# Kernel optimization log

Measured on AMD Instinct MI355X. Metric: run time of the kernel, lower is better.

## Reference

```python
import jax, jax.numpy as jnp
import numpy as np

B, F0, F1, E, C = 256, 39, 39, 16, 1  # batch, feature_nums[0], feature_nums[1], emb_size, w_channels
_ROWS, _COLS = np.tril_indices(F1, k=-1)  # strict lower triangle of (F1, F0); row-major order matches masked_select
I = _ROWS.shape[0]  # interaction_num = 741
BN_EPS = 1e-5


def setup_inputs() -> dict:
    key = jax.random.key(0)
    k1, k2, k3 = jax.random.split(key, 3)
    xi = jax.random.normal(k1, (B, F0, E), dtype=jnp.float32)
    xj = jax.random.normal(k2, (B, F1, E), dtype=jnp.float32)
    # W param is (1,1,C,E,E) in torch; keep the broadcastable core (C,E,E). Xavier-uniform bound.
    bound = float(np.sqrt(6.0 / (E + E)))
    W = jax.random.uniform(k3, (C, E, E), dtype=jnp.float32, minval=-bound, maxval=bound)
    gamma = jnp.ones((I,), dtype=jnp.float32)   # BatchNorm2d weight
    beta = jnp.zeros((I,), dtype=jnp.float32)   # BatchNorm2d bias
    return {"xi": xi, "xj": xj, "W": W, "gamma": gamma, "beta": beta}


def reference(xi, xj, W, gamma, beta):
    rows = jnp.asarray(_ROWS)
    cols = jnp.asarray(_COLS)
    # raw_cross[b,f1,f0,e1,e2] = xj[b,f1,e1] * xi[b,f0,e2]; only keep strict-lower-tri (f1,f0) pairs.
    # Compute triangular pairs directly instead of materializing the full (B,F1,F0,E,E) tensor.
    cross = xj[:, rows, :, None] * xi[:, cols, None, :]  # (B, I, E, E)
    # BatchNorm2d (training-mode batch stats, biased variance) over channels I
    mean = jnp.mean(cross, axis=(0, 2, 3), keepdims=True)            # (1, I, 1, 1)
    var = jnp.mean(jnp.square(cross - mean), axis=(0, 2, 3), keepdims=True)
    normed = (cross - mean) * jax.lax.rsqrt(var + BN_EPS)
    normed = normed * gamma[None, :, None, None] + beta[None, :, None, None]
    # broadcast multiply with W over w_channels, then transpose(1,2)
    out = normed[:, :, None, :, :] * W[None, None, :, :, :]          # (B, I, C, E, E)
    return jnp.transpose(out, (0, 2, 1, 3, 4))                        # (B, C, I, E, E)
```

## Files before the change

kernel.cpp:

```cpp
#include <hip/hip_runtime.h>
#include <math.h>

#define BB 256
#define FF 39
#define EE 16
#define II 741
#define BN_EPS 1e-5f
#define CPW 8
#define NB 4

typedef float vfloat4 __attribute__((ext_vector_type(4)));
typedef float vfloat2 __attribute__((ext_vector_type(2)));

struct OffTab { unsigned int v[II]; };
static constexpr OffTab make_off() {
    OffTab t{};
    int i = 0;
    for (int r = 1; r < FF; ++r)
        for (int c = 0; c < r; ++c) {
            t.v[i] = ((unsigned)(r * EE) << 16) | (unsigned)(c * EE);
            ++i;
        }
    return t;
}
__constant__ OffTab g_off = make_off();


__global__ __launch_bounds__(256) void
stats_kernel(const float* __restrict__ xi,
             const float* __restrict__ xj,
             const float* __restrict__ gamma,
             const float* __restrict__ beta,
             float* __restrict__ ws) {
    int wid = (blockIdx.x * blockDim.x + threadIdx.x) >> 6;
    int lane = threadIdx.x & 63;
    if (wid >= II) return;
    int i = wid;
    unsigned o = g_off.v[i];
    int joff = (int)(o >> 16);
    int coff = (int)(o & 0xffffu);

    float sumS = 0.f, sumQ = 0.f;
#pragma unroll
    for (int b = lane; b < BB; b += 64) {
        const vfloat4* xjr = reinterpret_cast<const vfloat4*>(xj + b * FF * EE + joff);
        const vfloat4* xic = reinterpret_cast<const vfloat4*>(xi + b * FF * EE + coff);
        float sj = 0.f, qj = 0.f, si = 0.f, qi = 0.f;
#pragma unroll
        for (int k = 0; k < 4; ++k) {
            vfloat4 vj = xjr[k];
            vfloat4 vi = xic[k];
            sj += vj.x + vj.y + vj.z + vj.w;
            qj += vj.x * vj.x + vj.y * vj.y + vj.z * vj.z + vj.w * vj.w;
            si += vi.x + vi.y + vi.z + vi.w;
            qi += vi.x * vi.x + vi.y * vi.y + vi.z * vi.z + vi.w * vi.w;
        }
        sumS += sj * si;
        sumQ += qj * qi;
    }
#pragma unroll
    for (int off = 32; off > 0; off >>= 1) {
        sumS += __shfl_xor(sumS, off);
        sumQ += __shfl_xor(sumQ, off);
    }
    if (lane == 0) {
        const float invN = 1.0f / (float)(BB * EE * EE);
        float mean = sumS * invN;
        float ex2 = sumQ * invN;
        float var = ex2 - mean * mean;
        float inv_std = 1.0f / sqrtf(var + BN_EPS);
        float a = gamma[i] * inv_std;
        float d = beta[i] - mean * a;
        vfloat2 e;
        e.x = a; e.y = d;
        reinterpret_cast<vfloat2*>(ws)[i] = e;
    }
}

__global__ __launch_bounds__(256) void
cross_bn_kernel(const float* __restrict__ xi,
                const float* __restrict__ xj,
                const float* __restrict__ W,
                const float* __restrict__ ws,
                float* __restrict__ out) {
    const vfloat2* T2 = reinterpret_cast<const vfloat2*>(ws);

    int t = threadIdx.x;
    int l = t & 63;
    int e1 = l >> 2;
    int e2q = l & 3;
    int wv = t >> 6;

    vfloat4 w4 = reinterpret_cast<const vfloat4*>(W)[e1 * 4 + e2q];

    int ibase = __builtin_amdgcn_readfirstlane(blockIdx.x * (4 * CPW) + wv * CPW);
    int b0 = blockIdx.y * NB;

    if (ibase + CPW <= II) {
        int joff[CPW], coff[CPW];
        float a[CPW], d[CPW];
#pragma unroll
        for (int k = 0; k < CPW; ++k) {
            unsigned o = g_off.v[ibase + k];
            joff[k] = (int)(o >> 16);
            coff[k] = (int)(o & 0xffffu);
            vfloat2 ad = T2[ibase + k];
            a[k] = ad.x; d[k] = ad.y;
        }
#pragma unroll
        for (int bb = 0; bb < NB; ++bb) {
            int b = b0 + bb;
            const float* xib = xi + b * FF * EE;
            const float* xjb = xj + b * FF * EE;
            float* outb = out + (size_t)b * (II * EE * EE) + (size_t)ibase * (EE * EE);
            float xjs[CPW];
            vfloat4 xi4[CPW];
#pragma unroll
            for (int k = 0; k < CPW; ++k) {
                xjs[k] = xjb[joff[k] + e1];
                xi4[k] = reinterpret_cast<const vfloat4*>(xib + coff[k])[e2q];
            }
#pragma unroll
            for (int k = 0; k < CPW; ++k) {
                vfloat4 o4;
                o4.x = (xjs[k] * xi4[k].x * a[k] + d[k]) * w4.x;
                o4.y = (xjs[k] * xi4[k].y * a[k] + d[k]) * w4.y;
                o4.z = (xjs[k] * xi4[k].z * a[k] + d[k]) * w4.z;
                o4.w = (xjs[k] * xi4[k].w * a[k] + d[k]) * w4.w;
                reinterpret_cast<vfloat4*>(outb + k * (EE * EE))[l] = o4;
            }
        }
    } else {
#pragma unroll
        for (int bb = 0; bb < NB; ++bb) {
            int b = b0 + bb;
            const float* xib = xi + b * FF * EE;
            const float* xjb = xj + b * FF * EE;
            float* outb = out + (size_t)b * (II * EE * EE);
            for (int k = 0; k < CPW; ++k) {
                int i = ibase + k;
                if (i >= II) break;
                unsigned o = g_off.v[i];
                int joff = (int)(o >> 16);
                int coff = (int)(o & 0xffffu);
                vfloat2 ad = T2[i];
                float xjs = xjb[joff + e1];
                vfloat4 xi4 = reinterpret_cast<const vfloat4*>(xib + coff)[e2q];
                vfloat4 o4;
                o4.x = (xjs * xi4.x * ad.x + ad.y) * w4.x;
                o4.y = (xjs * xi4.y * ad.x + ad.y) * w4.y;
                o4.z = (xjs * xi4.z * ad.x + ad.y) * w4.z;
                o4.w = (xjs * xi4.w * ad.x + ad.y) * w4.w;
                reinterpret_cast<vfloat4*>(outb + (size_t)i * (EE * EE))[l] = o4;
            }
        }
    }
}

extern "C" void kernel_launch(void* const* d_in, const int* in_sizes, int n_in,
                              void* d_out, int out_size, void* d_ws, size_t ws_size,
                              hipStream_t stream) {
    const float* xi = (const float*)d_in[0];
    const float* xj = (const float*)d_in[1];
    const float* W = (const float*)d_in[2];
    const float* gamma = (const float*)d_in[3];
    const float* beta = (const float*)d_in[4];
    float* out = (float*)d_out;
    float* ws = (float*)d_ws;

    stats_kernel<<<dim3((II * 64 + 255) / 256), 256, 0, stream>>>(xi, xj, gamma, beta, ws);
    const int CPB = 4 * CPW;
    cross_bn_kernel<<<dim3((II + CPB - 1) / CPB, BB / NB), 256, 0, stream>>>(xi, xj, W, ws, out);
}
```

Baseline: 43.14 us.

## Fuse stats and cross-BN kernels into one persistent kernel with grid barrier

Merges the BatchNorm statistics kernel and the output kernel into one persistent kernel of 512 blocks. Each wave first computes one channel's stats, then all blocks meet at an atomic-counter grid barrier before looping over the output tiles. This removes the second kernel launch and the gap between kernels, at the cost of a memset launch, a spin-wait barrier and reduced grid parallelism. The barrier assumes all 512 blocks are resident at the same time, which the launch bounds of 2 blocks per CU are meant to guarantee.

```diff
diff --git a/kernel.cpp b/kernel.cpp
--- a/kernel.cpp
+++ b/kernel.cpp
@@ -8,6 +8,10 @@
 #define BN_EPS 1e-5f
 #define CPW 8
 #define NB 4
+#define NCX 24
+#define NGY (BB / NB)
+#define NTILE (NCX * NGY)
+#define NBLK 512
 
 typedef float vfloat4 __attribute__((ext_vector_type(4)));
 typedef float vfloat2 __attribute__((ext_vector_type(2)));
@@ -25,133 +29,147 @@
 }
 __constant__ OffTab g_off = make_off();
 
-
-__global__ __launch_bounds__(256) void
-stats_kernel(const float* __restrict__ xi,
+__global__ __launch_bounds__(256, 2) void
+fused_kernel(const float* __restrict__ xi,
              const float* __restrict__ xj,
+             const float* __restrict__ W,
              const float* __restrict__ gamma,
              const float* __restrict__ beta,
-             float* __restrict__ ws) {
-    int wid = (blockIdx.x * blockDim.x + threadIdx.x) >> 6;
-    int lane = threadIdx.x & 63;
-    if (wid >= II) return;
-    int i = wid;
-    unsigned o = g_off.v[i];
-    int joff = (int)(o >> 16);
-    int coff = (int)(o & 0xffffu);
-
-    float sumS = 0.f, sumQ = 0.f;
-#pragma unroll
-    for (int b = lane; b < BB; b += 64) {
-        const vfloat4* xjr = reinterpret_cast<const vfloat4*>(xj + b * FF * EE + joff);
-        const vfloat4* xic = reinterpret_cast<const vfloat4*>(xi + b * FF * EE + coff);
-        float sj = 0.f, qj = 0.f, si = 0.f, qi = 0.f;
-#pragma unroll
-        for (int k = 0; k < 4; ++k) {
-            vfloat4 vj = xjr[k];
-            vfloat4 vi = xic[k];
-            sj += vj.x + vj.y + vj.z + vj.w;
-            qj += vj.x * vj.x + vj.y * vj.y + vj.z * vj.z + vj.w * vj.w;
-            si += vi.x + vi.y + vi.z + vi.w;
-            qi += vi.x * vi.x + vi.y * vi.y + vi.z * vi.z + vi.w * vi.w;
-        }
-        sumS += sj * si;
-        sumQ += qj * qi;
-    }
-#pragma unroll
-    for (int off = 32; off > 0; off >>= 1) {
-        sumS += __shfl_xor(sumS, off);
-        sumQ += __shfl_xor(sumQ, off);
-    }
-    if (lane == 0) {
-        const float invN = 1.0f / (float)(BB * EE * EE);
-        float mean = sumS * invN;
-        float ex2 = sumQ * invN;
-        float var = ex2 - mean * mean;
-        float inv_std = 1.0f / sqrtf(var + BN_EPS);
-        float a = gamma[i] * inv_std;
-        float d = beta[i] - mean * a;
-        vfloat2 e;
-        e.x = a; e.y = d;
-        reinterpret_cast<vfloat2*>(ws)[i] = e;
-    }
-}
-
-__global__ __launch_bounds__(256) void
-cross_bn_kernel(const float* __restrict__ xi,
-                const float* __restrict__ xj,
-                const float* __restrict__ W,
-                const float* __restrict__ ws,
-                float* __restrict__ out) {
-    const vfloat2* T2 = reinterpret_cast<const vfloat2*>(ws);
-
+             float* __restrict__ ws,
+             float* __restrict__ out) {
     int t = threadIdx.x;
     int l = t & 63;
+    int wv = t >> 6;
+
+    unsigned* counter = reinterpret_cast<unsigned*>(ws);
+    float* tbl = ws + 64;
+
+    int w = blockIdx.x * 4 + wv;
+    if (w < II) {
+        int i = w;
+        unsigned o = g_off.v[i];
+        int joff = (int)(o >> 16);
+        int coff = (int)(o & 0xffffu);
+
+        float sumS = 0.f, sumQ = 0.f;
+#pragma unroll
+        for (int b = l; b < BB; b += 64) {
+            const vfloat4* xjr = reinterpret_cast<const vfloat4*>(xj + b * FF * EE + joff);
+            const vfloat4* xic = reinterpret_cast<const vfloat4*>(xi + b * FF * EE + coff);
+            float sj = 0.f, qj = 0.f, si = 0.f, qi = 0.f;
+#pragma unroll
+            for (int k = 0; k < 4; ++k) {
+                vfloat4 vj = xjr[k];
+                vfloat4 vi = xic[k];
+                sj += vj.x + vj.y + vj.z + vj.w;
+                qj += vj.x * vj.x + vj.y * vj.y + vj.z * vj.z + vj.w * vj.w;
+                si += vi.x + vi.y + vi.z + vi.w;
+                qi += vi.x * vi.x + vi.y * vi.y + vi.z * vi.z + vi.w * vi.w;
+            }
+            sumS += sj * si;
+            sumQ += qj * qi;
+        }
+#pragma unroll
+        for (int off = 32; off > 0; off >>= 1) {
+            sumS += __shfl_xor(sumS, off);
+            sumQ += __shfl_xor(sumQ, off);
+        }
+        if (l == 0) {
+            const float invN = 1.0f / (float)(BB * EE * EE);
+            float mean = sumS * invN;
+            float ex2 = sumQ * invN;
+            float var = ex2 - mean * mean;
+            float inv_std = 1.0f / sqrtf(var + BN_EPS);
+            float a = gamma[i] * inv_std;
+            float d = beta[i] - mean * a;
+            vfloat2 e;
+            e.x = a; e.y = d;
+            reinterpret_cast<vfloat2*>(tbl)[i] = e;
+        }
+    }
+
+    __syncthreads();
+    if (t == 0) {
+        __threadfence();
+        __hip_atomic_fetch_add(counter, 1u, __ATOMIC_ACQ_REL, __HIP_MEMORY_SCOPE_AGENT);
+        while (__hip_atomic_load(counter, __ATOMIC_ACQUIRE, __HIP_MEMORY_SCOPE_AGENT) < NBLK) {
+            __builtin_amdgcn_s_sleep(2);
+        }
+        __threadfence();
+    }
+    __syncthreads();
+
+    const vfloat2* T2 = reinterpret_cast<const vfloat2*>(tbl);
     int e1 = l >> 2;
     int e2q = l & 3;
-    int wv = t >> 6;
 
     vfloat4 w4 = reinterpret_cast<const vfloat4*>(W)[e1 * 4 + e2q];
 
-    int ibase = __builtin_amdgcn_readfirstlane(blockIdx.x * (4 * CPW) + wv * CPW);
-    int b0 = blockIdx.y * NB;
+#pragma unroll
+    for (int rep = 0; rep < NTILE / NBLK; ++rep) {
+        int tile = blockIdx.x + rep * NBLK;
+        int cx = tile % NCX;
+        int gy = tile / NCX;
+        int ibase = __builtin_amdgcn_readfirstlane(cx * (4 * CPW) + wv * CPW);
+        int b0 = gy * NB;
 
-    if (ibase + CPW <= II) {
-        int joff[CPW], coff[CPW];
-        float a[CPW], d[CPW];
-#pragma unroll
-        for (int k = 0; k < CPW; ++k) {
-            unsigned o = g_off.v[ibase + k];
-            joff[k] = (int)(o >> 16);
-            coff[k] = (int)(o & 0xffffu);
-            vfloat2 ad = T2[ibase + k];
-            a[k] = ad.x; d[k] = ad.y;
-        }
-#pragma unroll
-        for (int bb = 0; bb < NB; ++bb) {
-            int b = b0 + bb;
-            const float* xib = xi + b * FF * EE;
-            const float* xjb = xj + b * FF * EE;
-            float* outb = out + (size_t)b * (II * EE * EE) + (size_t)ibase * (EE * EE);
-            float xjs[CPW];
-            vfloat4 xi4[CPW];
+        if (ibase + CPW <= II) {
+            int joff[CPW], coff[CPW];
+            float a[CPW], d[CPW];
 #pragma unroll
             for (int k = 0; k < CPW; ++k) {
-                xjs[k] = xjb[joff[k] + e1];
-                xi4[k] = reinterpret_cast<const vfloat4*>(xib + coff[k])[e2q];
+                unsigned o = g_off.v[ibase + k];
+                joff[k] = (int)(o >> 16);
+                coff[k] = (int)(o & 0xffffu);
+                vfloat2 ad = T2[ibase + k];
+                a[k] = ad.x; d[k] = ad.y;
             }
 #pragma unroll
-            for (int k = 0; k < CPW; ++k) {
-                vfloat4 o4;
-                o4.x = (xjs[k] * xi4[k].x * a[k] + d[k]) * w4.x;
-                o4.y = (xjs[k] * xi4[k].y * a[k] + d[k]) * w4.y;
-                o4.z = (xjs[k] * xi4[k].z * a[k] + d[k]) * w4.z;
-                o4.w = (xjs[k] * xi4[k].w * a[k] + d[k]) * w4.w;
-                reinterpret_cast<vfloat4*>(outb + k * (EE * EE))[l] = o4;
+            for (int bb = 0; bb < NB; ++bb) {
+                int b = b0 + bb;
+                const float* xib = xi + b * FF * EE;
+                const float* xjb = xj + b * FF * EE;
+                float* outb = out + (size_t)b * (II * EE * EE) + (size_t)ibase * (EE * EE);
+                float xjs[CPW];
+                vfloat4 xi4[CPW];
+#pragma unroll
+                for (int k = 0; k < CPW; ++k) {
+                    xjs[k] = xjb[joff[k] + e1];
+                    xi4[k] = reinterpret_cast<const vfloat4*>(xib + coff[k])[e2q];
+                }
+#pragma unroll
+                for (int k = 0; k < CPW; ++k) {
+                    vfloat4 o4;
+                    o4.x = (xjs[k] * xi4[k].x * a[k] + d[k]) * w4.x;
+                    o4.y = (xjs[k] * xi4[k].y * a[k] + d[k]) * w4.y;
+                    o4.z = (xjs[k] * xi4[k].z * a[k] + d[k]) * w4.z;
+                    o4.w = (xjs[k] * xi4[k].w * a[k] + d[k]) * w4.w;
+                    reinterpret_cast<vfloat4*>(outb + k * (EE * EE))[l] = o4;
+                }
             }
-        }
-    } else {
+        } else {
 #pragma unroll
-        for (int bb = 0; bb < NB; ++bb) {
-            int b = b0 + bb;
-            const float* xib = xi + b * FF * EE;
-            const float* xjb = xj + b * FF * EE;
-            float* outb = out + (size_t)b * (II * EE * EE);
-            for (int k = 0; k < CPW; ++k) {
-                int i = ibase + k;
-                if (i >= II) break;
-                unsigned o = g_off.v[i];
-                int joff = (int)(o >> 16);
-                int coff = (int)(o & 0xffffu);
-                vfloat2 ad = T2[i];
-                float xjs = xjb[joff + e1];
-                vfloat4 xi4 = reinterpret_cast<const vfloat4*>(xib + coff)[e2q];
-                vfloat4 o4;
-                o4.x = (xjs * xi4.x * ad.x + ad.y) * w4.x;
-                o4.y = (xjs * xi4.y * ad.x + ad.y) * w4.y;
-                o4.z = (xjs * xi4.z * ad.x + ad.y) * w4.z;
-                o4.w = (xjs * xi4.w * ad.x + ad.y) * w4.w;
-                reinterpret_cast<vfloat4*>(outb + (size_t)i * (EE * EE))[l] = o4;
+            for (int bb = 0; bb < NB; ++bb) {
+                int b = b0 + bb;
+                const float* xib = xi + b * FF * EE;
+                const float* xjb = xj + b * FF * EE;
+                float* outb = out + (size_t)b * (II * EE * EE);
+                for (int k = 0; k < CPW; ++k) {
+                    int i = ibase + k;
+                    if (i >= II) break;
+                    unsigned o = g_off.v[i];
+                    int joff = (int)(o >> 16);
+                    int coff = (int)(o & 0xffffu);
+                    vfloat2 ad = T2[i];
+                    float xjs = xjb[joff + e1];
+                    vfloat4 xi4 = reinterpret_cast<const vfloat4*>(xib + coff)[e2q];
+                    vfloat4 o4;
+                    o4.x = (xjs * xi4.x * ad.x + ad.y) * w4.x;
+                    o4.y = (xjs * xi4.y * ad.x + ad.y) * w4.y;
+                    o4.z = (xjs * xi4.z * ad.x + ad.y) * w4.z;
+                    o4.w = (xjs * xi4.w * ad.x + ad.y) * w4.w;
+                    reinterpret_cast<vfloat4*>(outb + (size_t)i * (EE * EE))[l] = o4;
+                }
             }
         }
     }
@@ -168,7 +186,6 @@
     float* out = (float*)d_out;
     float* ws = (float*)d_ws;
 
-    stats_kernel<<<dim3((II * 64 + 255) / 256), 256, 0, stream>>>(xi, xj, gamma, beta, ws);
-    const int CPB = 4 * CPW;
-    cross_bn_kernel<<<dim3((II + CPB - 1) / CPB, BB / NB), 256, 0, stream>>>(xi, xj, W, ws, out);
+    hipMemsetAsync(ws, 0, sizeof(unsigned), stream);
+    fused_kernel<<<dim3(NBLK), dim3(256), 0, stream>>>(xi, xj, W, gamma, beta, ws, out);
 }
```

New measurement: 161.9 us. +275.3%, slower.

## Replace 2D tiled output kernel with grid-stride linear wave loop

Applied to the files above, without the earlier changes.

Swaps the 2D grid (channel groups by batch groups, eight channels by four batches per wave) for a fixed grid of 2048 blocks. Each wave now strides over the flattened (batch, channel) index and writes one contiguous 1 KB output tile per iteration, so consecutive waves write consecutive memory. The aim is fully sequential store streams and less tail imbalance. In exchange, per-channel offsets and BN coefficients are no longer reused across batches, and each iteration adds an integer divide plus scalar-dependent loads.

```diff
diff --git a/kernel.cpp b/kernel.cpp
--- a/kernel.cpp
+++ b/kernel.cpp
@@ -6,8 +6,9 @@
 #define EE 16
 #define II 741
 #define BN_EPS 1e-5f
-#define CPW 8
-#define NB 4
+#define BFE (FF * EE)
+#define NROW (BB * FF)
+#define MAINBLK 2048
 
 typedef float vfloat4 __attribute__((ext_vector_type(4)));
 typedef float vfloat2 __attribute__((ext_vector_type(2)));
@@ -43,8 +44,8 @@
     float sumS = 0.f, sumQ = 0.f;
 #pragma unroll
     for (int b = lane; b < BB; b += 64) {
-        const vfloat4* xjr = reinterpret_cast<const vfloat4*>(xj + b * FF * EE + joff);
-        const vfloat4* xic = reinterpret_cast<const vfloat4*>(xi + b * FF * EE + coff);
+        const vfloat4* xjr = reinterpret_cast<const vfloat4*>(xj + b * BFE + joff);
+        const vfloat4* xic = reinterpret_cast<const vfloat4*>(xi + b * BFE + coff);
         float sj = 0.f, qj = 0.f, si = 0.f, qi = 0.f;
 #pragma unroll
         for (int k = 0; k < 4; ++k) {
@@ -78,7 +79,7 @@
 }
 
 __global__ __launch_bounds__(256) void
-cross_bn_kernel(const float* __restrict__ xi,
+cross_bn_linear(const float* __restrict__ xi,
                 const float* __restrict__ xj,
                 const float* __restrict__ W,
                 const float* __restrict__ ws,
@@ -89,71 +90,29 @@
     int l = t & 63;
     int e1 = l >> 2;
     int e2q = l & 3;
-    int wv = t >> 6;
 
     vfloat4 w4 = reinterpret_cast<const vfloat4*>(W)[e1 * 4 + e2q];
 
-    int ibase = __builtin_amdgcn_readfirstlane(blockIdx.x * (4 * CPW) + wv * CPW);
-    int b0 = blockIdx.y * NB;
+    const int NWAVES = MAINBLK * 4;
+    const int TOT = II * BB;
+    int wave = (blockIdx.x * 256 + t) >> 6;
 
-    if (ibase + CPW <= II) {
-        int joff[CPW], coff[CPW];
-        float a[CPW], d[CPW];
-#pragma unroll
-        for (int k = 0; k < CPW; ++k) {
-            unsigned o = g_off.v[ibase + k];
-            joff[k] = (int)(o >> 16);
-            coff[k] = (int)(o & 0xffffu);
-            vfloat2 ad = T2[ibase + k];
-            a[k] = ad.x; d[k] = ad.y;
-        }
-#pragma unroll
-        for (int bb = 0; bb < NB; ++bb) {
-            int b = b0 + bb;
-            const float* xib = xi + b * FF * EE;
-            const float* xjb = xj + b * FF * EE;
-            float* outb = out + (size_t)b * (II * EE * EE) + (size_t)ibase * (EE * EE);
-            float xjs[CPW];
-            vfloat4 xi4[CPW];
-#pragma unroll
-            for (int k = 0; k < CPW; ++k) {
-                xjs[k] = xjb[joff[k] + e1];
-                xi4[k] = reinterpret_cast<const vfloat4*>(xib + coff[k])[e2q];
-            }
-#pragma unroll
-            for (int k = 0; k < CPW; ++k) {
-                vfloat4 o4;
-                o4.x = (xjs[k] * xi4[k].x * a[k] + d[k]) * w4.x;
-                o4.y = (xjs[k] * xi4[k].y * a[k] + d[k]) * w4.y;
-                o4.z = (xjs[k] * xi4[k].z * a[k] + d[k]) * w4.z;
-                o4.w = (xjs[k] * xi4[k].w * a[k] + d[k]) * w4.w;
-                reinterpret_cast<vfloat4*>(outb + k * (EE * EE))[l] = o4;
-            }
-        }
-    } else {
-#pragma unroll
-        for (int bb = 0; bb < NB; ++bb) {
-            int b = b0 + bb;
-            const float* xib = xi + b * FF * EE;
-            const float* xjb = xj + b * FF * EE;
-            float* outb = out + (size_t)b * (II * EE * EE);
-            for (int k = 0; k < CPW; ++k) {
-                int i = ibase + k;
-                if (i >= II) break;
-                unsigned o = g_off.v[i];
-                int joff = (int)(o >> 16);
-                int coff = (int)(o & 0xffffu);
-                vfloat2 ad = T2[i];
-                float xjs = xjb[joff + e1];
-                vfloat4 xi4 = reinterpret_cast<const vfloat4*>(xib + coff)[e2q];
-                vfloat4 o4;
-                o4.x = (xjs * xi4.x * ad.x + ad.y) * w4.x;
-                o4.y = (xjs * xi4.y * ad.x + ad.y) * w4.y;
-                o4.z = (xjs * xi4.z * ad.x + ad.y) * w4.z;
-                o4.w = (xjs * xi4.w * ad.x + ad.y) * w4.w;
-                reinterpret_cast<vfloat4*>(outb + (size_t)i * (EE * EE))[l] = o4;
-            }
-        }
+#pragma unroll 2
+    for (int n = wave; n < TOT; n += NWAVES) {
+        int b = n / II;
+        int i = n - b * II;
+        unsigned o = g_off.v[i];
+        int joff = (int)(o >> 16);
+        int coff = (int)(o & 0xffffu);
+        vfloat2 ad = T2[i];
+        float xjs = xj[b * BFE + joff + e1];
+        vfloat4 xi4 = reinterpret_cast<const vfloat4*>(xi + b * BFE + coff)[e2q];
+        vfloat4 o4;
+        o4.x = (xjs * xi4.x * ad.x + ad.y) * w4.x;
+        o4.y = (xjs * xi4.y * ad.x + ad.y) * w4.y;
+        o4.z = (xjs * xi4.z * ad.x + ad.y) * w4.z;
+        o4.w = (xjs * xi4.w * ad.x + ad.y) * w4.w;
+        reinterpret_cast<vfloat4*>(out + (size_t)n * 256)[l] = o4;
     }
 }
 
@@ -169,6 +128,5 @@
     float* ws = (float*)d_ws;
 
     stats_kernel<<<dim3((II * 64 + 255) / 256), 256, 0, stream>>>(xi, xj, gamma, beta, ws);
-    const int CPB = 4 * CPW;
-    cross_bn_kernel<<<dim3((II + CPB - 1) / CPB, BB / NB), 256, 0, stream>>>(xi, xj, W, ws, out);
+    cross_bn_linear<<<dim3(MAINBLK), 256, 0, stream>>>(xi, xj, W, ws, out);
 }
```

Result: slower. 44.65 us (+3.5%).
